# Kernel tuning notes

Measured on AMD Instinct MI355X. Metric: run time of the kernel, lower is better.

The kernel has to match this reference:

```python
import jax, jax.numpy as jnp
import numpy as np

D = 128
P = 1.0
EPS_PD = 1e-6   # torch pairwise_distance eps
EPS_NORM = 1e-12  # torch F.normalize eps


def setup_inputs() -> dict:
    key = jax.random.key(0)
    k1, k2, k3, k4 = jax.random.split(key, 4)
    B = 8192
    triplet_idx = jax.random.randint(k1, (B, 5), 0, 1000, dtype=jnp.int64)
    entity_emb = jax.random.normal(k2, (500000, D), dtype=jnp.float32)
    relation_emb = jax.random.normal(k3, (1000, D), dtype=jnp.float32)
    time_transfer = jax.random.normal(k4, (1000, D * D), dtype=jnp.float32)
    return {"triplet_idx": triplet_idx, "entity_emb": entity_emb,
            "relation_emb": relation_emb, "time_transfer": time_transfer}


def _l2norm(x):
    n = jnp.sqrt(jnp.sum(x * x, axis=-1, keepdims=True))
    return x / jnp.maximum(n, EPS_NORM)


def reference(triplet_idx, entity_emb, relation_emb, time_transfer):
    h = entity_emb[triplet_idx[:, 0]]          # [B, D]
    r = relation_emb[triplet_idx[:, 1]]        # [B, D]
    t = entity_emb[triplet_idx[:, 2]]          # [B, D]
    B = h.shape[0]
    Ts = time_transfer[triplet_idx[:, 3]].reshape(B, D, D)
    Te = time_transfer[triplet_idx[:, 4]].reshape(B, D, D)
    M = Ts + Te                                # [B, D, D]
    h2 = _l2norm(jnp.einsum('bd,bde->be', h, M))
    t2 = _l2norm(jnp.einsum('bd,bde->be', t, M))
    diff = h2 + r - t2 + EPS_PD
    # torch pairwise_distance: (sum |diff|^p)^(1/p); p=1 -> sum abs
    score = jnp.sum(jnp.abs(diff) ** P, axis=-1) ** (1.0 / P)
    return score
```

## Files before the change

### kernel.cpp

```cpp
#include <hip/hip_runtime.h>

#define D 128
#define CAP_R 128

__global__ __launch_bounds__(256) void transe_time_kernel(
    const int* __restrict__ idx, const float* __restrict__ ent,
    const float* __restrict__ rel, const float* __restrict__ tt,
    float* __restrict__ out, int B)
{
    const int b = blockIdx.x;
    if (b >= B) return;
    const int tid = threadIdx.x;
    const int e4  = tid & 31;
    const int g   = tid >> 5;

    __shared__ float sh_h[D];
    __shared__ float sh_t[D];
    __shared__ float ph[8][D];
    __shared__ float pt[8][D];
    __shared__ float wred[8];

    const int hi = idx[b * 5 + 0];
    const int ri = idx[b * 5 + 1];
    const int ti = idx[b * 5 + 2];
    const int si = idx[b * 5 + 3];
    const int ei = idx[b * 5 + 4];

    if (tid < D) {
        sh_h[tid] = ent[(size_t)hi * D + tid];
        sh_t[tid] = ent[(size_t)ti * D + tid];
    }
    __syncthreads();

    const float4* __restrict__ Ts = (const float4*)(tt + (size_t)si * D * D);
    const float4* __restrict__ Te = (const float4*)(tt + (size_t)ei * D * D);

    float4 hacc = make_float4(0.f, 0.f, 0.f, 0.f);
    float4 tacc = make_float4(0.f, 0.f, 0.f, 0.f);

    #pragma unroll 4
    for (int d0 = 0; d0 < D; d0 += 8) {
        const int d = d0 + g;
        const float4 a = Ts[d * 32 + e4];
        const float4 c = Te[d * 32 + e4];
        const float hd = sh_h[d];
        const float td = sh_t[d];
        const float mx = a.x + c.x;
        const float my = a.y + c.y;
        const float mz = a.z + c.z;
        const float mw = a.w + c.w;
        hacc.x += hd * mx; hacc.y += hd * my; hacc.z += hd * mz; hacc.w += hd * mw;
        tacc.x += td * mx; tacc.y += td * my; tacc.z += td * mz; tacc.w += td * mw;
    }

    ((float4*)ph[g])[e4] = hacc;
    ((float4*)pt[g])[e4] = tacc;
    __syncthreads();

    float h2 = 0.f, t2 = 0.f;
    if (tid < D) {
        #pragma unroll
        for (int k = 0; k < 8; ++k) { h2 += ph[k][tid]; t2 += pt[k][tid]; }
    }
    float nh = h2 * h2;
    float nt = t2 * t2;
    #pragma unroll
    for (int off = 32; off; off >>= 1) {
        nh += __shfl_down(nh, off, 64);
        nt += __shfl_down(nt, off, 64);
    }
    const int wv = tid >> 6;
    if ((tid & 63) == 0) { wred[wv * 2] = nh; wred[wv * 2 + 1] = nt; }
    __syncthreads();
    const float NH = wred[0] + wred[2] + wred[4] + wred[6];
    const float NT2 = wred[1] + wred[3] + wred[5] + wred[7];
    const float rnh = 1.0f / fmaxf(sqrtf(NH), 1e-12f);
    const float rnt = 1.0f / fmaxf(sqrtf(NT2), 1e-12f);

    float v = 0.f;
    if (tid < D) {
        const float rr = rel[(size_t)ri * D + tid];
        v = fabsf(h2 * rnh + rr - t2 * rnt + 1e-6f);
    }
    #pragma unroll
    for (int off = 32; off; off >>= 1) v += __shfl_down(v, off, 64);
    __syncthreads();
    if ((tid & 63) == 0) wred[wv] = v;
    __syncthreads();
    if (tid == 0) out[b] = wred[0] + wred[1] + wred[2] + wred[3];
}


__global__ __launch_bounds__(1024) void zero_cnt_kernel(int* __restrict__ cnt, int NT)
{
    const int t = threadIdx.x;
    if (t < NT) cnt[t] = 0;
}

__global__ __launch_bounds__(256) void scatter_kernel(
    const int* __restrict__ idx, int* __restrict__ cnt,
    int2* __restrict__ rowsbuf, int B)
{
    const int i = blockIdx.x * blockDim.x + threadIdx.x;
    const int stride = gridDim.x * blockDim.x;
    for (int b = i; b < B; b += stride) {
        const int h_eid = idx[b * 5 + 0];
        const int t_eid = idx[b * 5 + 2];
        #pragma unroll
        for (int slot = 0; slot < 2; ++slot) {
            const int u = idx[b * 5 + 3 + slot];
            const int p = atomicAdd(&cnt[u], 2);
            if (p + 1 < CAP_R) {
                rowsbuf[u * CAP_R + p]     = make_int2(h_eid, (b * 2 + 0) * 2 + slot);
                rowsbuf[u * CAP_R + p + 1] = make_int2(t_eid, (b * 2 + 1) * 2 + slot);
            }
        }
    }
}

__device__ __forceinline__ void fma4(float4& a, float s, const float4& v) {
    a.x += s * v.x; a.y += s * v.y; a.z += s * v.z; a.w += s * v.w;
}

template<int NG>
__device__ __forceinline__ void compute_store(
    const float* __restrict__ Tc, const float (*__restrict__ Esh)[D + 4],
    const int* __restrict__ Dsh, float* __restrict__ P,
    const int col0, const int rh, const int my_rows)
{
    float4 acc[NG];
    #pragma unroll
    for (int k = 0; k < NG; ++k) acc[k] = make_float4(0.f, 0.f, 0.f, 0.f);

    #pragma unroll 2
    for (int d4 = 0; d4 < D; d4 += 4) {
        const float* tp = Tc + (size_t)d4 * D;
        const float4 t0 = *(const float4*)(tp);
        const float4 t1 = *(const float4*)(tp + D);
        const float4 t2 = *(const float4*)(tp + 2 * D);
        const float4 t3 = *(const float4*)(tp + 3 * D);
        #pragma unroll
        for (int k = 0; k < NG; ++k) {
            const float4 e = *(const float4*)&Esh[rh + 8 * k][d4];
            fma4(acc[k], e.x, t0); fma4(acc[k], e.y, t1);
            fma4(acc[k], e.z, t2); fma4(acc[k], e.w, t3);
        }
    }

    #pragma unroll
    for (int k = 0; k < NG; ++k) {
        const int r = rh + 8 * k;
        if (r < my_rows) {
            float* dst = P + (size_t)Dsh[r] * D + col0;
            *(float4*)dst = acc[k];
        }
    }
}

__global__ __launch_bounds__(256) void matvec_kernel(
    const float* __restrict__ ent, const float* __restrict__ tt,
    const int* __restrict__ cnt, const int2* __restrict__ rowsbuf,
    float* __restrict__ P)
{
    const int u = blockIdx.x;
    int n_rows = cnt[u];
    if (n_rows > CAP_R) n_rows = CAP_R;
    const int base = u * CAP_R;
    const int tid = threadIdx.x;

    const int w    = tid >> 6;
    const int lane = tid & 63;
    const int c8   = lane & 7;
    const int rh   = lane >> 3;
    const int col0 = w * 32 + c8 * 4;

    __shared__ float Esh[32][D + 4];
    __shared__ int   Dsh[32];
    const float* __restrict__ T = tt + (size_t)u * (D * D);
    const float* __restrict__ Tc = T + col0;

    for (int rr0 = blockIdx.y * 32; rr0 < n_rows; rr0 += 64) {
        const int my_rows = min(32, n_rows - rr0);

        {
            const int r  = tid >> 3;
            const int j8 = tid & 7;
            if (r < my_rows) {
                const int2 rec = rowsbuf[base + rr0 + r];
                const float* src = ent + (size_t)rec.x * D + j8 * 16;
                const float4 v0 = *(const float4*)(src);
                const float4 v1 = *(const float4*)(src + 4);
                const float4 v2 = *(const float4*)(src + 8);
                const float4 v3 = *(const float4*)(src + 12);
                float* drow = &Esh[r][j8 * 16];
                *(float4*)(drow)      = v0;
                *(float4*)(drow + 4)  = v1;
                *(float4*)(drow + 8)  = v2;
                *(float4*)(drow + 12) = v3;
                if (j8 == 0) Dsh[r] = rec.y;
            }
        }
        __syncthreads();

        const int ng = (my_rows + 7) >> 3;
        switch (ng) {
            case 1: compute_store<1>(Tc, Esh, Dsh, P, col0, rh, my_rows); break;
            case 2: compute_store<2>(Tc, Esh, Dsh, P, col0, rh, my_rows); break;
            case 3: compute_store<3>(Tc, Esh, Dsh, P, col0, rh, my_rows); break;
            default: compute_store<4>(Tc, Esh, Dsh, P, col0, rh, my_rows); break;
        }
        __syncthreads();
    }
}

__global__ __launch_bounds__(256) void score_kernel(
    const int* __restrict__ idx, const float* __restrict__ rel,
    const float* __restrict__ P, float* __restrict__ out, int B)
{
    const int tid = threadIdx.x;
    const int b = blockIdx.x * 4 + (tid >> 6);
    const int l = tid & 63;
    if (b >= B) return;

    const int ri = idx[b * 5 + 1];
    const float* ph = P + (size_t)(b * 2 + 0) * 2 * D;
    const float* pt = P + (size_t)(b * 2 + 1) * 2 * D;

    const float h0 = ph[l]      + ph[D + l];
    const float h1 = ph[64 + l] + ph[D + 64 + l];
    const float t0 = pt[l]      + pt[D + l];
    const float t1 = pt[64 + l] + pt[D + 64 + l];

    float nh = h0 * h0 + h1 * h1;
    float nt = t0 * t0 + t1 * t1;
    #pragma unroll
    for (int off = 32; off; off >>= 1) {
        nh += __shfl_down(nh, off, 64);
        nt += __shfl_down(nt, off, 64);
    }
    nh = __shfl(nh, 0, 64);
    nt = __shfl(nt, 0, 64);
    const float rnh = 1.0f / fmaxf(sqrtf(nh), 1e-12f);
    const float rnt = 1.0f / fmaxf(sqrtf(nt), 1e-12f);
    const float r0 = rel[(size_t)ri * D + l];
    const float r1 = rel[(size_t)ri * D + 64 + l];
    float v = fabsf(h0 * rnh + r0 - t0 * rnt + 1e-6f)
            + fabsf(h1 * rnh + r1 - t1 * rnt + 1e-6f);
    #pragma unroll
    for (int off = 32; off; off >>= 1) v += __shfl_down(v, off, 64);
    if (l == 0) out[b] = v;
}

extern "C" void kernel_launch(void* const* d_in, const int* in_sizes, int n_in,
                              void* d_out, int out_size, void* d_ws, size_t ws_size,
                              hipStream_t stream) {
    const int*   idx = (const int*)d_in[0];
    const float* ent = (const float*)d_in[1];
    const float* rel = (const float*)d_in[2];
    const float* tt  = (const float*)d_in[3];
    float* out = (float*)d_out;
    const int B  = in_sizes[0] / 5;
    const int NT = in_sizes[3] / (D * D);

    const size_t CNT_OFF  = 0;
    const size_t ROWS_OFF = 8192;
    const size_t ROWS_BYTES = (size_t)NT * CAP_R * sizeof(int2);
    const size_t P_OFF  = (ROWS_OFF + ROWS_BYTES + 255) & ~(size_t)255;
    const size_t need   = P_OFF + (size_t)B * 2 * 2 * D * sizeof(float);

    if (ws_size < need || NT > 1024) {
        transe_time_kernel<<<dim3(B), dim3(256), 0, stream>>>(idx, ent, rel, tt, out, B);
        return;
    }

    char* ws = (char*)d_ws;
    int*  cnt     = (int*)(ws + CNT_OFF);
    int2* rowsbuf = (int2*)(ws + ROWS_OFF);
    float* P      = (float*)(ws + P_OFF);

    zero_cnt_kernel<<<dim3(1),           dim3(1024), 0, stream>>>(cnt, NT);
    scatter_kernel <<<dim3(32),          dim3(256),  0, stream>>>(idx, cnt, rowsbuf, B);
    matvec_kernel  <<<dim3(NT, 2),       dim3(256),  0, stream>>>(ent, tt, cnt, rowsbuf, P);
    score_kernel   <<<dim3((B + 3) / 4), dim3(256),  0, stream>>>(idx, rel, P, out, B);
}
```

Baseline: 51.49 us.

## Replace global bucketing with per-block index scan inside matvec kernel

```diff
diff --git a/kernel.cpp b/kernel.cpp
--- a/kernel.cpp
+++ b/kernel.cpp
@@ -1,7 +1,7 @@
 #include <hip/hip_runtime.h>
 
 #define D 128
-#define CAP_R 128
+#define MAXR 96
 
 __global__ __launch_bounds__(256) void transe_time_kernel(
     const int* __restrict__ idx, const float* __restrict__ ent,
@@ -91,33 +91,6 @@
 }
 
 
-__global__ __launch_bounds__(1024) void zero_cnt_kernel(int* __restrict__ cnt, int NT)
-{
-    const int t = threadIdx.x;
-    if (t < NT) cnt[t] = 0;
-}
-
-__global__ __launch_bounds__(256) void scatter_kernel(
-    const int* __restrict__ idx, int* __restrict__ cnt,
-    int2* __restrict__ rowsbuf, int B)
-{
-    const int i = blockIdx.x * blockDim.x + threadIdx.x;
-    const int stride = gridDim.x * blockDim.x;
-    for (int b = i; b < B; b += stride) {
-        const int h_eid = idx[b * 5 + 0];
-        const int t_eid = idx[b * 5 + 2];
-        #pragma unroll
-        for (int slot = 0; slot < 2; ++slot) {
-            const int u = idx[b * 5 + 3 + slot];
-            const int p = atomicAdd(&cnt[u], 2);
-            if (p + 1 < CAP_R) {
-                rowsbuf[u * CAP_R + p]     = make_int2(h_eid, (b * 2 + 0) * 2 + slot);
-                rowsbuf[u * CAP_R + p + 1] = make_int2(t_eid, (b * 2 + 1) * 2 + slot);
-            }
-        }
-    }
-}
-
 __device__ __forceinline__ void fma4(float4& a, float s, const float4& v) {
     a.x += s * v.x; a.y += s * v.y; a.z += s * v.z; a.w += s * v.w;
 }
@@ -125,7 +98,7 @@
 template<int NG>
 __device__ __forceinline__ void compute_store(
     const float* __restrict__ Tc, const float (*__restrict__ Esh)[D + 4],
-    const int* __restrict__ Dsh, float* __restrict__ P,
+    const int2* __restrict__ rows_chunk, float* __restrict__ P,
     const int col0, const int rh, const int my_rows)
 {
     float4 acc[NG];
@@ -151,22 +124,42 @@
     for (int k = 0; k < NG; ++k) {
         const int r = rh + 8 * k;
         if (r < my_rows) {
-            float* dst = P + (size_t)Dsh[r] * D + col0;
+            float* dst = P + (size_t)rows_chunk[r].y * D + col0;
             *(float4*)dst = acc[k];
         }
     }
 }
 
-__global__ __launch_bounds__(256) void matvec_kernel(
-    const float* __restrict__ ent, const float* __restrict__ tt,
-    const int* __restrict__ cnt, const int2* __restrict__ rowsbuf,
-    float* __restrict__ P)
-{
-    const int u = blockIdx.x;
-    int n_rows = cnt[u];
-    if (n_rows > CAP_R) n_rows = CAP_R;
-    const int base = u * CAP_R;
-    const int tid = threadIdx.x;
+__global__ __launch_bounds__(256) void matvec_scan_kernel(
+    const int* __restrict__ idx, const float* __restrict__ ent,
+    const float* __restrict__ tt, float* __restrict__ P, int B)
+{
+    const int u    = blockIdx.x;
+    const int half = blockIdx.y;
+    const int tid  = threadIdx.x;
+
+    __shared__ int2 s_rows[MAXR];
+    __shared__ int  s_m;
+    __shared__ float Esh[32][D + 4];
+    if (tid == 0) s_m = 0;
+    __syncthreads();
+
+    #pragma unroll 4
+    for (int b = tid; b < B; b += 256) {
+        if (idx[b * 5 + 3 + half] == u) {
+            const int he = idx[b * 5 + 0];
+            const int te = idx[b * 5 + 2];
+            const int p = atomicAdd(&s_m, 2);
+            if (p + 1 < MAXR) {
+                s_rows[p]     = make_int2(he, b * 4 + 0 + half);
+                s_rows[p + 1] = make_int2(te, b * 4 + 2 + half);
+            }
+        }
+    }
+    __syncthreads();
+    int n_rows = s_m;
+    if (n_rows > MAXR) n_rows = MAXR;
+    if (n_rows == 0) return;
 
     const int w    = tid >> 6;
     const int lane = tid & 63;
@@ -174,20 +167,17 @@
     const int rh   = lane >> 3;
     const int col0 = w * 32 + c8 * 4;
 
-    __shared__ float Esh[32][D + 4];
-    __shared__ int   Dsh[32];
-    const float* __restrict__ T = tt + (size_t)u * (D * D);
-    const float* __restrict__ Tc = T + col0;
-
-    for (int rr0 = blockIdx.y * 32; rr0 < n_rows; rr0 += 64) {
+    const float* __restrict__ Tc = tt + (size_t)u * (D * D) + col0;
+
+    for (int rr0 = 0; rr0 < n_rows; rr0 += 32) {
         const int my_rows = min(32, n_rows - rr0);
 
         {
             const int r  = tid >> 3;
             const int j8 = tid & 7;
             if (r < my_rows) {
-                const int2 rec = rowsbuf[base + rr0 + r];
-                const float* src = ent + (size_t)rec.x * D + j8 * 16;
+                const int eid = s_rows[rr0 + r].x;
+                const float* src = ent + (size_t)eid * D + j8 * 16;
                 const float4 v0 = *(const float4*)(src);
                 const float4 v1 = *(const float4*)(src + 4);
                 const float4 v2 = *(const float4*)(src + 8);
@@ -197,17 +187,16 @@
                 *(float4*)(drow + 4)  = v1;
                 *(float4*)(drow + 8)  = v2;
                 *(float4*)(drow + 12) = v3;
-                if (j8 == 0) Dsh[r] = rec.y;
             }
         }
         __syncthreads();
 
         const int ng = (my_rows + 7) >> 3;
         switch (ng) {
-            case 1: compute_store<1>(Tc, Esh, Dsh, P, col0, rh, my_rows); break;
-            case 2: compute_store<2>(Tc, Esh, Dsh, P, col0, rh, my_rows); break;
-            case 3: compute_store<3>(Tc, Esh, Dsh, P, col0, rh, my_rows); break;
-            default: compute_store<4>(Tc, Esh, Dsh, P, col0, rh, my_rows); break;
+            case 1: compute_store<1>(Tc, Esh, &s_rows[rr0], P, col0, rh, my_rows); break;
+            case 2: compute_store<2>(Tc, Esh, &s_rows[rr0], P, col0, rh, my_rows); break;
+            case 3: compute_store<3>(Tc, Esh, &s_rows[rr0], P, col0, rh, my_rows); break;
+            default: compute_store<4>(Tc, Esh, &s_rows[rr0], P, col0, rh, my_rows); break;
         }
         __syncthreads();
     }
@@ -223,8 +212,8 @@
     if (b >= B) return;
 
     const int ri = idx[b * 5 + 1];
-    const float* ph = P + (size_t)(b * 2 + 0) * 2 * D;
-    const float* pt = P + (size_t)(b * 2 + 1) * 2 * D;
+    const float* ph = P + (size_t)(b * 4 + 0) * D;
+    const float* pt = P + (size_t)(b * 4 + 2) * D;
 
     const float h0 = ph[l]      + ph[D + l];
     const float h1 = ph[64 + l] + ph[D + 64 + l];
@@ -262,24 +251,15 @@
     const int B  = in_sizes[0] / 5;
     const int NT = in_sizes[3] / (D * D);
 
-    const size_t CNT_OFF  = 0;
-    const size_t ROWS_OFF = 8192;
-    const size_t ROWS_BYTES = (size_t)NT * CAP_R * sizeof(int2);
-    const size_t P_OFF  = (ROWS_OFF + ROWS_BYTES + 255) & ~(size_t)255;
-    const size_t need   = P_OFF + (size_t)B * 2 * 2 * D * sizeof(float);
-
-    if (ws_size < need || NT > 1024) {
+    const size_t need = (size_t)B * 4 * D * sizeof(float);
+
+    if (ws_size < need) {
         transe_time_kernel<<<dim3(B), dim3(256), 0, stream>>>(idx, ent, rel, tt, out, B);
         return;
     }
 
-    char* ws = (char*)d_ws;
-    int*  cnt     = (int*)(ws + CNT_OFF);
-    int2* rowsbuf = (int2*)(ws + ROWS_OFF);
-    float* P      = (float*)(ws + P_OFF);
-
-    zero_cnt_kernel<<<dim3(1),           dim3(1024), 0, stream>>>(cnt, NT);
-    scatter_kernel <<<dim3(32),          dim3(256),  0, stream>>>(idx, cnt, rowsbuf, B);
-    matvec_kernel  <<<dim3(NT, 2),       dim3(256),  0, stream>>>(ent, tt, cnt, rowsbuf, P);
-    score_kernel   <<<dim3((B + 3) / 4), dim3(256),  0, stream>>>(idx, rel, P, out, B);
-}
+    float* P = (float*)d_ws;
+
+    matvec_scan_kernel<<<dim3(NT, 2),       dim3(256), 0, stream>>>(idx, ent, tt, P, B);
+    score_kernel      <<<dim3((B + 3) / 4), dim3(256), 0, stream>>>(idx, rel, P, out, B);
+}
```

Result: slower. 65.23 us (+26.7%).

## Split matvec reduction dimension across blockIdx.y instead of splitting rows

Applied to the files above, without the earlier changes.

```diff
diff --git a/kernel.cpp b/kernel.cpp
--- a/kernel.cpp
+++ b/kernel.cpp
@@ -111,8 +111,8 @@
             const int u = idx[b * 5 + 3 + slot];
             const int p = atomicAdd(&cnt[u], 2);
             if (p + 1 < CAP_R) {
-                rowsbuf[u * CAP_R + p]     = make_int2(h_eid, (b * 2 + 0) * 2 + slot);
-                rowsbuf[u * CAP_R + p + 1] = make_int2(t_eid, (b * 2 + 1) * 2 + slot);
+                rowsbuf[u * CAP_R + p]     = make_int2(h_eid, b * 4 + 0 + slot);
+                rowsbuf[u * CAP_R + p + 1] = make_int2(t_eid, b * 4 + 2 + slot);
             }
         }
     }
@@ -124,16 +124,16 @@
 
 template<int NG>
 __device__ __forceinline__ void compute_store(
-    const float* __restrict__ Tc, const float (*__restrict__ Esh)[D + 4],
+    const float* __restrict__ Tc, const float (*__restrict__ Esh)[68],
     const int* __restrict__ Dsh, float* __restrict__ P,
-    const int col0, const int rh, const int my_rows)
+    const int col0, const int rh, const int my_rows, const int dh)
 {
     float4 acc[NG];
     #pragma unroll
     for (int k = 0; k < NG; ++k) acc[k] = make_float4(0.f, 0.f, 0.f, 0.f);
 
     #pragma unroll 2
-    for (int d4 = 0; d4 < D; d4 += 4) {
+    for (int d4 = 0; d4 < 64; d4 += 4) {
         const float* tp = Tc + (size_t)d4 * D;
         const float4 t0 = *(const float4*)(tp);
         const float4 t1 = *(const float4*)(tp + D);
@@ -151,7 +151,7 @@
     for (int k = 0; k < NG; ++k) {
         const int r = rh + 8 * k;
         if (r < my_rows) {
-            float* dst = P + (size_t)Dsh[r] * D + col0;
+            float* dst = P + (size_t)((Dsh[r] << 1) | dh) * D + col0;
             *(float4*)dst = acc[k];
         }
     }
@@ -162,8 +162,10 @@
     const int* __restrict__ cnt, const int2* __restrict__ rowsbuf,
     float* __restrict__ P)
 {
-    const int u = blockIdx.x;
+    const int u  = blockIdx.x;
+    const int dh = blockIdx.y;
     int n_rows = cnt[u];
+    if (n_rows == 0) return;
     if (n_rows > CAP_R) n_rows = CAP_R;
     const int base = u * CAP_R;
     const int tid = threadIdx.x;
@@ -174,40 +176,43 @@
     const int rh   = lane >> 3;
     const int col0 = w * 32 + c8 * 4;
 
-    __shared__ float Esh[32][D + 4];
-    __shared__ int   Dsh[32];
-    const float* __restrict__ T = tt + (size_t)u * (D * D);
-    const float* __restrict__ Tc = T + col0;
-
-    for (int rr0 = blockIdx.y * 32; rr0 < n_rows; rr0 += 64) {
-        const int my_rows = min(32, n_rows - rr0);
+    __shared__ float Esh[64][68];
+    __shared__ int   Dsh[64];
+    const float* __restrict__ Tc = tt + (size_t)u * (D * D) + (size_t)dh * 64 * D + col0;
+
+    for (int rr0 = 0; rr0 < n_rows; rr0 += 64) {
+        const int my_rows = min(64, n_rows - rr0);
 
         {
-            const int r  = tid >> 3;
-            const int j8 = tid & 7;
+            const int r = tid >> 2;
+            const int q = tid & 3;
             if (r < my_rows) {
                 const int2 rec = rowsbuf[base + rr0 + r];
-                const float* src = ent + (size_t)rec.x * D + j8 * 16;
+                const float* src = ent + (size_t)rec.x * D + dh * 64 + q * 16;
                 const float4 v0 = *(const float4*)(src);
                 const float4 v1 = *(const float4*)(src + 4);
                 const float4 v2 = *(const float4*)(src + 8);
                 const float4 v3 = *(const float4*)(src + 12);
-                float* drow = &Esh[r][j8 * 16];
+                float* drow = &Esh[r][q * 16];
                 *(float4*)(drow)      = v0;
                 *(float4*)(drow + 4)  = v1;
                 *(float4*)(drow + 8)  = v2;
                 *(float4*)(drow + 12) = v3;
-                if (j8 == 0) Dsh[r] = rec.y;
+                if (q == 0) Dsh[r] = rec.y;
             }
         }
         __syncthreads();
 
         const int ng = (my_rows + 7) >> 3;
         switch (ng) {
-            case 1: compute_store<1>(Tc, Esh, Dsh, P, col0, rh, my_rows); break;
-            case 2: compute_store<2>(Tc, Esh, Dsh, P, col0, rh, my_rows); break;
-            case 3: compute_store<3>(Tc, Esh, Dsh, P, col0, rh, my_rows); break;
-            default: compute_store<4>(Tc, Esh, Dsh, P, col0, rh, my_rows); break;
+            case 1: compute_store<1>(Tc, Esh, Dsh, P, col0, rh, my_rows, dh); break;
+            case 2: compute_store<2>(Tc, Esh, Dsh, P, col0, rh, my_rows, dh); break;
+            case 3: compute_store<3>(Tc, Esh, Dsh, P, col0, rh, my_rows, dh); break;
+            case 4: compute_store<4>(Tc, Esh, Dsh, P, col0, rh, my_rows, dh); break;
+            case 5: compute_store<5>(Tc, Esh, Dsh, P, col0, rh, my_rows, dh); break;
+            case 6: compute_store<6>(Tc, Esh, Dsh, P, col0, rh, my_rows, dh); break;
+            case 7: compute_store<7>(Tc, Esh, Dsh, P, col0, rh, my_rows, dh); break;
+            default: compute_store<8>(Tc, Esh, Dsh, P, col0, rh, my_rows, dh); break;
         }
         __syncthreads();
     }
@@ -223,13 +228,16 @@
     if (b >= B) return;
 
     const int ri = idx[b * 5 + 1];
-    const float* ph = P + (size_t)(b * 2 + 0) * 2 * D;
-    const float* pt = P + (size_t)(b * 2 + 1) * 2 * D;
-
-    const float h0 = ph[l]      + ph[D + l];
-    const float h1 = ph[64 + l] + ph[D + 64 + l];
-    const float t0 = pt[l]      + pt[D + l];
-    const float t1 = pt[64 + l] + pt[D + 64 + l];
+    const float* pb = P + (size_t)b * 8 * D;
+
+    float h0 = 0.f, h1 = 0.f, t0 = 0.f, t1 = 0.f;
+    #pragma unroll
+    for (int j = 0; j < 4; ++j) {
+        h0 += pb[j * D + l];
+        h1 += pb[j * D + 64 + l];
+        t0 += pb[(4 + j) * D + l];
+        t1 += pb[(4 + j) * D + 64 + l];
+    }
 
     float nh = h0 * h0 + h1 * h1;
     float nt = t0 * t0 + t1 * t1;
@@ -266,7 +274,7 @@
     const size_t ROWS_OFF = 8192;
     const size_t ROWS_BYTES = (size_t)NT * CAP_R * sizeof(int2);
     const size_t P_OFF  = (ROWS_OFF + ROWS_BYTES + 255) & ~(size_t)255;
-    const size_t need   = P_OFF + (size_t)B * 2 * 2 * D * sizeof(float);
+    const size_t need   = P_OFF + (size_t)B * 8 * D * sizeof(float);
 
     if (ws_size < need || NT > 1024) {
         transe_time_kernel<<<dim3(B), dim3(256), 0, stream>>>(idx, ent, rel, tt, out, B);
```

Result: faster. 50.22 us (-2.5%).
